# Kernel optimization log

Measured on AMD Instinct MI355X. Metric: run time of the kernel, lower is better.

The kernel has to match this reference:

```python
import jax, jax.numpy as jnp
import numpy as np

B, T, C, H = 8, 2048, 1024, 128


def setup_inputs() -> dict:
    key = jax.random.key(0)
    k1, k2, k3, k4 = jax.random.split(key, 4)
    x = jax.random.normal(k1, (B, T, C), dtype=jnp.float32)
    # torch nn.Linear(n_embed, head_size, bias=False) weights, stored as [C, H] for x @ W
    scale = 1.0 / np.sqrt(C)
    Wk = jax.random.normal(k2, (C, H), dtype=jnp.float32) * scale
    Wq = jax.random.normal(k3, (C, H), dtype=jnp.float32) * scale
    Wv = jax.random.normal(k4, (C, H), dtype=jnp.float32) * scale
    return {"x": x, "Wk": Wk, "Wq": Wq, "Wv": Wv}


def reference(x, Wk, Wq, Wv):
    # Faithful translation of Head.forward (dropout = identity in eval mode).
    Bx, Tx, Cx = x.shape
    k = x @ Wk  # [B,T,H]
    q = x @ Wq  # [B,T,H]
    v = x @ Wv  # [B,T,H]
    # NOTE: original scales by C**-0.5 (n_embed), not head_size**-0.5.
    scores = jnp.einsum('bth,bsh->bts', q, k) * (Cx ** -0.5)  # [B,T,T]
    causal = jnp.tril(jnp.ones((Tx, Tx), dtype=bool))  # tril buffer
    scores = jnp.where(causal, scores, -jnp.inf)
    weights = jax.nn.softmax(scores, axis=-1)
    out = jnp.einsum('bts,bsh->bth', weights, v)  # [B,T,H]
    return out
```

## Files before the change

### kernel.cpp

```cpp
#include <hip/hip_runtime.h>
#include <type_traits>

#define Bn 8
#define Tn 2048
#define Cn 1024
#define Hn 128
#define Mn (Bn*Tn)

typedef __attribute__((ext_vector_type(4))) float f32x4;
typedef __attribute__((ext_vector_type(2))) float f32x2;
typedef __attribute__((ext_vector_type(16))) float f32x16;
typedef __attribute__((ext_vector_type(8))) short s16x8;
typedef __attribute__((ext_vector_type(4))) int i32x4;
typedef __attribute__((ext_vector_type(2))) int i32x2;
typedef unsigned int u32;

__device__ __forceinline__ unsigned short f2bf(float f) {
  union { float f; unsigned u; } v; v.f = f;
  unsigned r = v.u + 0x7FFFu + ((v.u >> 16) & 1u);
  return (unsigned short)(r >> 16);
}

__device__ __forceinline__ float bf2f(unsigned s) {
  return __builtin_bit_cast(float, s << 16);
}

__device__ __forceinline__ unsigned cvtpk(float lo, float hi) {
  unsigned r;
  asm("v_cvt_pk_bf16_f32 %0, %1, %2" : "=v"(r) : "v"(lo), "v"(hi));
  return r;
}

__device__ __forceinline__ i32x2 swap32(int a, int b) {
#if __has_builtin(__builtin_amdgcn_permlane32_swap)
  return __builtin_amdgcn_permlane32_swap(a, b, false, false);
#else
  int ax = __shfl_xor(a, 32), bx = __shfl_xor(b, 32);
  i32x2 r;
  r[0] = (threadIdx.x & 32) ? bx : a;
  r[1] = (threadIdx.x & 32) ? b : ax;
  return r;
#endif
}

__device__ __forceinline__ void gl_lds16(const void* g, void* l) {
  __builtin_amdgcn_global_load_lds((const __attribute__((address_space(1))) u32*)g,
                                   (__attribute__((address_space(3))) u32*)l, 16, 0, 0);
}

__global__ __launch_bounds__(256) void prep_wt(const float* __restrict__ Wq,
                                               const float* __restrict__ Wk,
                                               const float* __restrict__ Wv,
                                               unsigned short* __restrict__ Wt) {
  __shared__ float tile[64][33];
  const int w = blockIdx.z;
  const float* W = (w == 0) ? Wq : (w == 1) ? Wk : Wv;
  const float scale = (w == 0) ? 0.03125f : 1.0f;
  const int c0 = blockIdx.x * 64, h0 = blockIdx.y * 32;
  const int tid = threadIdx.x;
  const int hl = tid & 31, cg = tid >> 5;
#pragma unroll
  for (int i = 0; i < 8; i++) {
    int cl = cg * 8 + i;
    tile[cl][hl] = W[(c0 + cl) * Hn + h0 + hl];
  }
  __syncthreads();
  const int cl2 = tid & 63, hg = tid >> 6;
#pragma unroll
  for (int i = 0; i < 8; i++) {
    int hl2 = hg * 8 + i;
    Wt[(size_t)(w * Hn + h0 + hl2) * Cn + c0 + cl2] = f2bf(tile[cl2][hl2] * scale);
  }
}

__global__ __launch_bounds__(512, 1) void proj_fused(const float* __restrict__ x,
                                                     const unsigned short* __restrict__ Wt,
                                                     unsigned short* __restrict__ qkv) {
  __shared__ __align__(16) unsigned short Abuf[2][64 * 64];
  __shared__ __align__(16) unsigned short Bbuf[2][384 * 64];
  const int tid = threadIdx.x;
  const int lane = tid & 63, wv = tid >> 6;
  const int wm = wv >> 2, wn = wv & 3;
  const int l31 = lane & 31, hi = lane >> 5;
  const int bm = blockIdx.x * 64;
  const int phase = (blockIdx.x >> 3) & 15;

  const int ar = tid >> 3;
  const int as = tid & 7;

  f32x16 acc[3];
#pragma unroll
  for (int i = 0; i < 3; i++)
#pragma unroll
    for (int r = 0; r < 16; r++) acc[i][r] = 0.f;

  auto slice = [&](int u) { return ((u + phase) & 15) * 64; };

  auto stageB = [&](int buf, int kk) {
#pragma unroll
    for (int i = 0; i < 6; i++) {
      int r0 = wv * 48 + i * 8;
      int n = r0 + (lane >> 3);
      const unsigned short* src = Wt + (size_t)n * Cn + kk + (((lane & 7) ^ (n & 7)) << 3);
      gl_lds16(src, &Bbuf[buf][r0 * 64]);
    }
  };
  auto loadA = [&](int kk, float4& v0, float4& v1) {
    const float* g = x + (size_t)(bm + ar) * Cn + kk + as * 8;
    v0 = *(const float4*)g;
    v1 = *(const float4*)(g + 4);
  };
  auto writeA = [&](int buf, float4 v0, float4 v1) {
    i32x4 w = {(int)cvtpk(v0.x, v0.y), (int)cvtpk(v0.z, v0.w),
               (int)cvtpk(v1.x, v1.y), (int)cvtpk(v1.z, v1.w)};
    *(i32x4*)&Abuf[buf][ar * 64 + ((as ^ (ar & 7)) << 3)] = w;
  };

  float4 pa0, pa1;

  {
    float4 p0, p1;
    loadA(slice(0), p0, p1);
    loadA(slice(1), pa0, pa1);
    stageB(0, slice(0));
    writeA(0, p0, p1);
  }

  const int arow = wm * 32 + l31;

  auto body = [&](int t, auto PC) {
    constexpr int P = decltype(PC)::value;
    const bool more1 = (t + 1 < 16);
    const bool more2 = (t + 2 < 16);
    __builtin_amdgcn_s_barrier();
    if (more1) writeA(P ^ 1, pa0, pa1);
    if (more2) loadA(slice(t + 2), pa0, pa1);
    if (more1) {
      stageB(P ^ 1, slice(t + 1));
      asm volatile("s_waitcnt vmcnt(8) lgkmcnt(0)" ::: "memory");
    } else {
      asm volatile("s_waitcnt vmcnt(0) lgkmcnt(0)" ::: "memory");
    }
    __builtin_amdgcn_s_barrier();
    __builtin_amdgcn_sched_barrier(0);
    s16x8 aF[4];
#pragma unroll
    for (int ks = 0; ks < 4; ks++)
      aF[ks] = *(const s16x8*)&Abuf[P][arow * 64 + (((ks * 2 + hi) ^ (arow & 7)) << 3)];
    __builtin_amdgcn_s_setprio(1);
#pragma unroll
    for (int ks = 0; ks < 4; ks++)
#pragma unroll
      for (int ni = 0; ni < 3; ni++) {
        int brow = wn * 96 + ni * 32 + l31;
        s16x8 bF = *(const s16x8*)&Bbuf[P][brow * 64 + (((ks * 2 + hi) ^ (brow & 7)) << 3)];
        acc[ni] = __builtin_amdgcn_mfma_f32_32x32x16_bf16(aF[ks], bF, acc[ni], 0, 0, 0);
      }
    __builtin_amdgcn_s_setprio(0);
  };

  for (int t = 0; t < 16; t += 2) {
    body(t, std::integral_constant<int, 0>{});
    body(t + 1, std::integral_constant<int, 1>{});
  }

#pragma unroll
  for (int ni = 0; ni < 3; ni++) {
    const int cb = wn * 3 + ni;
    if (cb < 8) {
      const int w = cb >> 2;
      const int h = (cb & 3) * 32 + l31;
      unsigned short* o = qkv + (size_t)w * ((size_t)Mn * Hn);
#pragma unroll
      for (int r = 0; r < 16; r++) {
        int m = bm + wm * 32 + (r & 3) + 8 * (r >> 2) + 4 * hi;
        o[(size_t)m * Hn + h] = f2bf(acc[ni][r]);
      }
    } else {
      const int h = (cb - 8) * 32 + l31;
      const int bb = bm >> 11;
      const int tl0 = (bm & 2047) + wm * 32;
      unsigned short* vt = qkv + (size_t)2 * Mn * Hn + (size_t)bb * (Hn * Tn) + (size_t)h * Tn;
#pragma unroll
      for (int r = 0; r < 16; r++)
        vt[tl0 + (r & 3) + 8 * (r >> 2) + 4 * hi] = f2bf(acc[ni][r]);
    }
  }
}

__global__ __launch_bounds__(256, 2) void attn_fwd(const unsigned short* __restrict__ qkv,
                                                   unsigned short* __restrict__ o_part,
                                                   float* __restrict__ ml,
                                                   int sshift) {
  __shared__ __align__(16) unsigned short Kl[2][64 * 128];
  __shared__ __align__(16) unsigned short Vl[2][128 * 64];

  const int bid = blockIdx.x;
  const int b = bid & 7;
  const int r = bid >> 3;
  const int jj = r & 15;
  const int sp = r >> 4;
  const int S = 1 << sshift;
  const int j = (S > 1 && sp >= (S >> 1)) ? (15 - jj) : jj;
  const int s = sp;

  const int tid = threadIdx.x;
  const int lane = tid & 63, wv = tid >> 6;
  const int l31 = lane & 31, hi = lane >> 5;

  const unsigned short* qb  = qkv + (size_t)b * (Tn * Hn);
  const unsigned short* kb  = qkv + (size_t)(Mn * Hn) + (size_t)b * (Tn * Hn);
  const unsigned short* vtb = qkv + (size_t)2 * (Mn * Hn) + (size_t)b * (Hn * Tn);

  const int qrow0 = j * 128 + wv * 32;
  const int qg = qrow0 + l31;

  const int ntt = (j + 1) * 2;
  const int tlo = (s * ntt) >> sshift;
  const int thi = ((s + 1) * ntt) >> sshift;

  f32x16 oT[4];
#pragma unroll
  for (int i = 0; i < 4; i++)
#pragma unroll
    for (int q = 0; q < 16; q++) oT[i][q] = 0.f;
  float m_ = -1e30f, l_ = 0.f;

  auto stage = [&](int buf, int tile) {
    const int kvb0 = tile * 64;
#pragma unroll
    for (int i = 0; i < 4; i++) {
      int r0 = wv * 16 + i * 4;
      int row = r0 + (lane >> 4);
      int ch = lane & 15;
      const unsigned short* src = kb + (size_t)(kvb0 + row) * Hn + ((ch ^ (row & 7)) << 3);
      gl_lds16(src, &Kl[buf][r0 * 128]);
    }
#pragma unroll
    for (int i = 0; i < 4; i++) {
      int r0 = wv * 32 + i * 8;
      int row = r0 + (lane >> 3);
      int ch = lane & 7;
      const unsigned short* src = vtb + (size_t)row * Tn + kvb0 + ((ch ^ (row & 7)) << 3);
      gl_lds16(src, &Vl[buf][r0 * 64]);
    }
  };

  if (tlo < thi) {
    s16x8 qB[8];
#pragma unroll
    for (int hs = 0; hs < 8; hs++)
      qB[hs] = *(const s16x8*)(qb + (size_t)qg * Hn + hs * 16 + hi * 8);

    stage(0, tlo);
    int buf = 0;

    for (int t = tlo; t < thi; t++) {
      if (t + 1 < thi) {
        stage(buf ^ 1, t + 1);
        asm volatile("s_waitcnt vmcnt(8)" ::: "memory");
      } else {
        asm volatile("s_waitcnt vmcnt(0)" ::: "memory");
      }
      __builtin_amdgcn_s_barrier();
      __builtin_amdgcn_sched_barrier(0);
      const int kvb = t * 64;
      if (kvb < qrow0 + 32) {
        const unsigned short* Kb = &Kl[buf][0];
        f32x16 sv0, sv1;
#pragma unroll
        for (int q = 0; q < 16; q++) { sv0[q] = 0.f; sv1[q] = 0.f; }
        __builtin_amdgcn_s_setprio(1);
        {
          const int row = l31;
#pragma unroll
          for (int hs = 0; hs < 8; hs++) {
            s16x8 kf = *(const s16x8*)&Kb[row * 128 + (((hs * 2 + hi) ^ (row & 7)) << 3)];
            sv0 = __builtin_amdgcn_mfma_f32_32x32x16_bf16(kf, qB[hs], sv0, 0, 0, 0);
          }
        }
        {
          const int row = 32 + l31;
#pragma unroll
          for (int hs = 0; hs < 8; hs++) {
            s16x8 kf = *(const s16x8*)&Kb[row * 128 + (((hs * 2 + hi) ^ (row & 7)) << 3)];
            sv1 = __builtin_amdgcn_mfma_f32_32x32x16_bf16(kf, qB[hs], sv1, 0, 0, 0);
          }
        }
        __builtin_amdgcn_s_setprio(0);
        if (kvb + 63 > qrow0) {
#pragma unroll
          for (int q = 0; q < 16; q++) {
            int kr = (q & 3) + 8 * (q >> 2) + 4 * hi;
            if (kvb + kr > qg) sv0[q] = -1e30f;
            if (kvb + 32 + kr > qg) sv1[q] = -1e30f;
          }
        }
        float om = sv0[0];
#pragma unroll
        for (int q = 1; q < 16; q++) om = fmaxf(om, sv0[q]);
#pragma unroll
        for (int q = 0; q < 16; q++) om = fmaxf(om, sv1[q]);
        i32x2 mx = swap32(__builtin_bit_cast(int, om), __builtin_bit_cast(int, om));
        float pm = __builtin_bit_cast(float, hi ? mx[0] : mx[1]);
        float tmax = fmaxf(om, pm);
        if (__any(tmax > m_ + 8.f)) {
          float mn = fmaxf(m_, tmax);
          float sc = __expf(m_ - mn);
          m_ = mn; l_ *= sc;
#pragma unroll
          for (int i = 0; i < 4; i++)
#pragma unroll
            for (int q = 0; q < 16; q++) oT[i][q] *= sc;
        }
        float osum = 0.f;
#pragma unroll
        for (int q = 0; q < 16; q++) { sv0[q] = __expf(sv0[q] - m_); osum += sv0[q]; }
#pragma unroll
        for (int q = 0; q < 16; q++) { sv1[q] = __expf(sv1[q] - m_); osum += sv1[q]; }
        i32x2 sx = swap32(__builtin_bit_cast(int, osum), __builtin_bit_cast(int, osum));
        float psum = __builtin_bit_cast(float, hi ? sx[0] : sx[1]);
        l_ += osum + psum;
        s16x8 pB[4];
        {
          unsigned PK[8];
#pragma unroll
          for (int n = 0; n < 8; n++) PK[n] = cvtpk(sv0[2 * n], sv0[2 * n + 1]);
          i32x2 e0 = swap32((int)PK[0], (int)PK[2]);
          i32x2 e1 = swap32((int)PK[1], (int)PK[3]);
          i32x2 e2 = swap32((int)PK[4], (int)PK[6]);
          i32x2 e3 = swap32((int)PK[5], (int)PK[7]);
          i32x4 w0 = {e0[0], e1[0], e0[1], e1[1]};
          i32x4 w1 = {e2[0], e3[0], e2[1], e3[1]};
          pB[0] = __builtin_bit_cast(s16x8, w0);
          pB[1] = __builtin_bit_cast(s16x8, w1);
        }
        {
          unsigned PK[8];
#pragma unroll
          for (int n = 0; n < 8; n++) PK[n] = cvtpk(sv1[2 * n], sv1[2 * n + 1]);
          i32x2 e0 = swap32((int)PK[0], (int)PK[2]);
          i32x2 e1 = swap32((int)PK[1], (int)PK[3]);
          i32x2 e2 = swap32((int)PK[4], (int)PK[6]);
          i32x2 e3 = swap32((int)PK[5], (int)PK[7]);
          i32x4 w0 = {e0[0], e1[0], e0[1], e1[1]};
          i32x4 w1 = {e2[0], e3[0], e2[1], e3[1]};
          pB[2] = __builtin_bit_cast(s16x8, w0);
          pB[3] = __builtin_bit_cast(s16x8, w1);
        }
        __builtin_amdgcn_s_setprio(1);
#pragma unroll
        for (int hsl = 0; hsl < 4; hsl++) {
          const int row = hsl * 32 + l31;
#pragma unroll
          for (int ks = 0; ks < 4; ks++) {
            s16x8 vf = *(const s16x8*)&Vl[buf][row * 64 + (((ks * 2 + hi) ^ (row & 7)) << 3)];
            oT[hsl] = __builtin_amdgcn_mfma_f32_32x32x16_bf16(vf, pB[ks], oT[hsl], 0, 0, 0);
          }
        }
        __builtin_amdgcn_s_setprio(0);
      }
      __builtin_amdgcn_s_barrier();
      buf ^= 1;
    }
  }

  unsigned short* orow = o_part + (size_t)s * ((size_t)Mn * Hn) + (size_t)(b * Tn + qg) * Hn;
#pragma unroll
  for (int hsl = 0; hsl < 4; hsl++)
#pragma unroll
    for (int g = 0; g < 4; g++) {
      unsigned p0 = cvtpk(oT[hsl][4 * g + 0], oT[hsl][4 * g + 1]);
      unsigned p1 = cvtpk(oT[hsl][4 * g + 2], oT[hsl][4 * g + 3]);
      i32x2 st = {(int)p0, (int)p1};
      *(i32x2*)(orow + hsl * 32 + g * 8 + hi * 4) = st;
    }
  if (lane < 32) {
    f32x2 w = {m_, l_};
    *(f32x2*)(ml + (size_t)s * (Mn * 2) + (size_t)(b * Tn + qg) * 2) = w;
  }
}

__global__ __launch_bounds__(256) void combine(const unsigned short* __restrict__ o_part,
                                               const float* __restrict__ ml,
                                               float* __restrict__ out, int S) {
  const int q = blockIdx.x * 4 + (threadIdx.x >> 6);
  const int p = threadIdx.x & 63;
  float M = -1e30f;
  for (int s = 0; s < S; s++) M = fmaxf(M, ml[(size_t)s * (Mn * 2) + q * 2]);
  float L = 0.f, a0 = 0.f, a1 = 0.f;
  for (int s = 0; s < S; s++) {
    float ms = ml[(size_t)s * (Mn * 2) + q * 2];
    float ls = ml[(size_t)s * (Mn * 2) + q * 2 + 1];
    float w = __expf(ms - M);
    L += ls * w;
    u32 v = *(const u32*)(o_part + (size_t)s * ((size_t)Mn * Hn) + (size_t)q * Hn + p * 2);
    a0 += bf2f(v & 0xffffu) * w;
    a1 += bf2f(v >> 16) * w;
  }
  float2 o = {a0 / L, a1 / L};
  *(float2*)(out + (size_t)q * Hn + p * 2) = o;
}

extern "C" void kernel_launch(void* const* d_in, const int* in_sizes, int n_in,
                              void* d_out, int out_size, void* d_ws, size_t ws_size,
                              hipStream_t stream) {
  const float* x  = (const float*)d_in[0];
  const float* Wk = (const float*)d_in[1];
  const float* Wq = (const float*)d_in[2];
  const float* Wv = (const float*)d_in[3];
  float* out = (float*)d_out;

  char* ws = (char*)d_ws;
  const size_t wt_b  = 786432;
  const size_t qkv_b = (size_t)3 * Mn * Hn * 2;
  const size_t base  = wt_b + qkv_b;
  const size_t per   = (size_t)Mn * Hn * 2 + (size_t)Mn * 8;
  int sshift = (ws_size >= base + 4 * per) ? 2 : (ws_size >= base + 2 * per) ? 1 : 0;
  const int S = 1 << sshift;

  unsigned short* Wt  = (unsigned short*)ws;
  unsigned short* qkv = (unsigned short*)(ws + wt_b);
  unsigned short* o_part = (unsigned short*)(ws + base);
  float* mlp = (float*)(ws + base + (size_t)S * Mn * Hn * 2);

  prep_wt<<<dim3(16, 4, 3), 256, 0, stream>>>(Wq, Wk, Wv, Wt);
  proj_fused<<<256, 512, 0, stream>>>(x, Wt, qkv);
  attn_fwd<<<128 * S, 256, 0, stream>>>(qkv, o_part, mlp, sshift);
  combine<<<Mn / 4, 256, 0, stream>>>(o_part, mlp, out, S);
}
```

Before: 64.84 us.

## Retile QKV projection to 128x192 blocks with register-resident A fragments

The projection GEMM now uses 128-row by 192-column tiles over a 2D grid and a K step of 128, replacing the single 64x384 tile. The A operand (fp32 x) is loaded straight from global memory into registers in MFMA fragment layout and packed to bf16 there, so the A LDS buffer and its write pass are removed. The aim is to cut LDS traffic and halve the number of K iterations and barriers. In exchange each thread holds 32 float4 registers for the double-buffered A prefetch, which raises register pressure, and each x row is read by both column blocks.

Result: slower. 85.09 us (+31.2%).

```diff
diff --git a/kernel.cpp b/kernel.cpp
--- a/kernel.cpp
+++ b/kernel.cpp
@@ -76,17 +76,16 @@
 __global__ __launch_bounds__(512, 1) void proj_fused(const float* __restrict__ x,
                                                      const unsigned short* __restrict__ Wt,
                                                      unsigned short* __restrict__ qkv) {
-  __shared__ __align__(16) unsigned short Abuf[2][64 * 64];
-  __shared__ __align__(16) unsigned short Bbuf[2][384 * 64];
+  __shared__ __align__(16) unsigned short Bbuf[2][192 * 128];
   const int tid = threadIdx.x;
   const int lane = tid & 63, wv = tid >> 6;
-  const int wm = wv >> 2, wn = wv & 3;
+  const int wm = wv >> 1, wn = wv & 1;
   const int l31 = lane & 31, hi = lane >> 5;
-  const int bm = blockIdx.x * 64;
-  const int phase = (blockIdx.x >> 3) & 15;
-
-  const int ar = tid >> 3;
-  const int as = tid & 7;
+  const int bm = blockIdx.x * 128;
+  const int bn = blockIdx.y * 192;
+  const int phase = (blockIdx.x >> 3) & 7;
+
+  const float* xrow = x + (size_t)(bm + wm * 32 + l31) * Cn;
 
   f32x16 acc[3];
 #pragma unroll
@@ -94,79 +93,74 @@
 #pragma unroll
     for (int r = 0; r < 16; r++) acc[i][r] = 0.f;
 
-  auto slice = [&](int u) { return ((u + phase) & 15) * 64; };
+  auto slice = [&](int u) { return ((u + phase) & 7) * 128; };
 
   auto stageB = [&](int buf, int kk) {
 #pragma unroll
     for (int i = 0; i < 6; i++) {
-      int r0 = wv * 48 + i * 8;
-      int n = r0 + (lane >> 3);
-      const unsigned short* src = Wt + (size_t)n * Cn + kk + (((lane & 7) ^ (n & 7)) << 3);
-      gl_lds16(src, &Bbuf[buf][r0 * 64]);
+      int r0 = wv * 24 + i * 4;
+      int r = r0 + (lane >> 4);
+      int c = (lane & 15) ^ (r & 15);
+      const unsigned short* src = Wt + (size_t)(bn + r) * Cn + kk + c * 8;
+      gl_lds16(src, &Bbuf[buf][r0 * 128]);
     }
   };
-  auto loadA = [&](int kk, float4& v0, float4& v1) {
-    const float* g = x + (size_t)(bm + ar) * Cn + kk + as * 8;
-    v0 = *(const float4*)g;
-    v1 = *(const float4*)(g + 4);
+  auto loadA = [&](int kk, float4* R) {
+#pragma unroll
+    for (int ks = 0; ks < 8; ks++) {
+      const float* g = xrow + kk + ks * 16 + hi * 8;
+      R[2 * ks]     = *(const float4*)g;
+      R[2 * ks + 1] = *(const float4*)(g + 4);
+    }
   };
-  auto writeA = [&](int buf, float4 v0, float4 v1) {
-    i32x4 w = {(int)cvtpk(v0.x, v0.y), (int)cvtpk(v0.z, v0.w),
-               (int)cvtpk(v1.x, v1.y), (int)cvtpk(v1.z, v1.w)};
-    *(i32x4*)&Abuf[buf][ar * 64 + ((as ^ (ar & 7)) << 3)] = w;
+  auto packA = [&](const float4* R, s16x8* aF) {
+#pragma unroll
+    for (int ks = 0; ks < 8; ks++) {
+      i32x4 w = {(int)cvtpk(R[2 * ks].x, R[2 * ks].y),
+                 (int)cvtpk(R[2 * ks].z, R[2 * ks].w),
+                 (int)cvtpk(R[2 * ks + 1].x, R[2 * ks + 1].y),
+                 (int)cvtpk(R[2 * ks + 1].z, R[2 * ks + 1].w)};
+      aF[ks] = __builtin_bit_cast(s16x8, w);
+    }
   };
 
-  float4 pa0, pa1;
-
-  {
-    float4 p0, p1;
-    loadA(slice(0), p0, p1);
-    loadA(slice(1), pa0, pa1);
-    stageB(0, slice(0));
-    writeA(0, p0, p1);
-  }
-
-  const int arow = wm * 32 + l31;
+  float4 RA[16], RB[16];
+  loadA(slice(0), RA);
+  stageB(0, slice(0));
 
   auto body = [&](int t, auto PC) {
     constexpr int P = decltype(PC)::value;
-    const bool more1 = (t + 1 < 16);
-    const bool more2 = (t + 2 < 16);
-    __builtin_amdgcn_s_barrier();
-    if (more1) writeA(P ^ 1, pa0, pa1);
-    if (more2) loadA(slice(t + 2), pa0, pa1);
-    if (more1) {
-      stageB(P ^ 1, slice(t + 1));
-      asm volatile("s_waitcnt vmcnt(8) lgkmcnt(0)" ::: "memory");
-    } else {
-      asm volatile("s_waitcnt vmcnt(0) lgkmcnt(0)" ::: "memory");
-    }
+    const bool more = (t < 7);
+    s16x8 aF[8];
+    if constexpr (P == 0) packA(RA, aF); else packA(RB, aF);
+    asm volatile("s_waitcnt vmcnt(0)" ::: "memory");
     __builtin_amdgcn_s_barrier();
     __builtin_amdgcn_sched_barrier(0);
-    s16x8 aF[4];
-#pragma unroll
-    for (int ks = 0; ks < 4; ks++)
-      aF[ks] = *(const s16x8*)&Abuf[P][arow * 64 + (((ks * 2 + hi) ^ (arow & 7)) << 3)];
+    if (more) {
+      stageB(P ^ 1, slice(t + 1));
+      if constexpr (P == 0) loadA(slice(t + 1), RB); else loadA(slice(t + 1), RA);
+    }
     __builtin_amdgcn_s_setprio(1);
 #pragma unroll
-    for (int ks = 0; ks < 4; ks++)
+    for (int ks = 0; ks < 8; ks++)
 #pragma unroll
       for (int ni = 0; ni < 3; ni++) {
-        int brow = wn * 96 + ni * 32 + l31;
-        s16x8 bF = *(const s16x8*)&Bbuf[P][brow * 64 + (((ks * 2 + hi) ^ (brow & 7)) << 3)];
+        const int brow = wn * 96 + ni * 32 + l31;
+        const int c = (ks * 2 + hi) ^ (brow & 15);
+        s16x8 bF = *(const s16x8*)&Bbuf[P][brow * 128 + c * 8];
         acc[ni] = __builtin_amdgcn_mfma_f32_32x32x16_bf16(aF[ks], bF, acc[ni], 0, 0, 0);
       }
     __builtin_amdgcn_s_setprio(0);
   };
 
-  for (int t = 0; t < 16; t += 2) {
+  for (int t = 0; t < 8; t += 2) {
     body(t, std::integral_constant<int, 0>{});
     body(t + 1, std::integral_constant<int, 1>{});
   }
 
 #pragma unroll
   for (int ni = 0; ni < 3; ni++) {
-    const int cb = wn * 3 + ni;
+    const int cb = blockIdx.y * 6 + wn * 3 + ni;
     if (cb < 8) {
       const int w = cb >> 2;
       const int h = (cb & 3) * 32 + l31;
@@ -425,7 +419,7 @@
   float* mlp = (float*)(ws + base + (size_t)S * Mn * Hn * 2);
 
   prep_wt<<<dim3(16, 4, 3), 256, 0, stream>>>(Wq, Wk, Wv, Wt);
-  proj_fused<<<256, 512, 0, stream>>>(x, Wt, qkv);
+  proj_fused<<<dim3(128, 2), 512, 0, stream>>>(x, Wt, qkv);
   attn_fwd<<<128 * S, 256, 0, stream>>>(qkv, o_part, mlp, sshift);
   combine<<<Mn / 4, 256, 0, stream>>>(o_part, mlp, out, S);
 }
```
